# Kernel optimization log

Hardware: AMD Instinct MI355X
Metric: run time of the kernel (lower is better)

The kernel has to match this reference:

```python
import jax, jax.numpy as jnp
import numpy as np

N = 8192
IN_DIM = 512
OUT_DIM = 512


def setup_inputs() -> dict:
    key = jax.random.key(0)
    kA, kX, k1, k2, k3, k4 = jax.random.split(key, 6)
    A = jax.random.uniform(kA, (N, N), dtype=jnp.float32)  # strictly positive -> nonzero triu
    X = jax.random.normal(kX, (N, IN_DIM), dtype=jnp.float32)
    s = 1.0 / np.sqrt(IN_DIM)
    W1 = jax.random.uniform(k1, (OUT_DIM, IN_DIM), minval=-s, maxval=s, dtype=jnp.float32)  # fc
    b1 = jax.random.uniform(k2, (OUT_DIM,), minval=-s, maxval=s, dtype=jnp.float32)
    W2 = jax.random.uniform(k3, (OUT_DIM, IN_DIM), minval=-s, maxval=s, dtype=jnp.float32)  # fc2
    b2 = jax.random.uniform(k4, (OUT_DIM,), minval=-s, maxval=s, dtype=jnp.float32)
    return {"A": A, "X": X, "W1": W1, "b1": b1, "W2": W2, "b2": b2}


def reference(A, X, W1, b1, W2, b2):
    n = A.shape[0]
    # strictly upper-triangular mask (diagonal=1); with uniform(0,1) fill all these
    # entries are nonzero, so torch.nonzero selects exactly them: m = n(n-1)/2 values.
    triu_mask = jnp.triu(jnp.ones((n, n), dtype=bool), k=1)
    m = n * (n - 1) // 2
    # torch.median = lower median = sorted[(m-1)//2]; pad non-triu entries with +inf
    vals = jnp.where(triu_mask, A, jnp.inf).reshape(-1)
    median_value = jnp.sort(vals)[(m - 1) // 2]
    # A[A < median] = 0
    A_thr = jnp.where(A < median_value, jnp.zeros((), A.dtype), A)
    A_norm = jax.nn.softmax(A_thr, axis=-1)
    fcX = X @ W1.T + b1    # [N, out_dim]
    fc2X = X @ W2.T + b2   # [N, out_dim]
    out = jax.nn.leaky_relu(0.1 * fc2X + 0.9 * (A_norm @ fcX), negative_slope=0.01)
    return out
```

## Files before the change

### kernel.cpp

```cpp
#include <hip/hip_runtime.h>

#define DEVI __device__ __forceinline__

typedef __attribute__((ext_vector_type(8))) short short8;
typedef __attribute__((ext_vector_type(4))) float f32x4;

static constexpr int NN = 8192;
static constexpr int DD = 512;
static constexpr unsigned LOB = 0x3EFE0000u;
static constexpr unsigned HIB = 0x3F020000u;
static constexpr long long K_RANK = 16775167LL;

static constexpr size_t WS_HIST = 0;
static constexpr size_t WS_CNT  = 1048576;
static constexpr size_t WS_MED  = 1048832;
static constexpr size_t WS_XB   = 2097152;
static constexpr size_t WS_W1B  = WS_XB  + (size_t)NN * DD * 2;
static constexpr size_t WS_W2B  = WS_W1B + (size_t)DD * DD * 2;
static constexpr size_t WS_FCXT = WS_W2B + (size_t)DD * DD * 2;
static constexpr size_t WS_FC2  = WS_FCXT + (size_t)NN * DD * 2;
static constexpr size_t WS_UP   = WS_FC2 + (size_t)NN * DD * 4;
static constexpr size_t WS_ZP   = WS_UP  + (size_t)4 * NN * DD * 2;

DEVI unsigned short f2bf(float f) {
  unsigned u = __float_as_uint(f);
  u += 0x7fffu + ((u >> 16) & 1u);
  return (unsigned short)(u >> 16);
}
DEVI float bf2f(unsigned short h) { return __uint_as_float(((unsigned)h) << 16); }
DEVI int swz(int row, int kq) { return kq ^ ((row >> 1) & 3); }

DEVI void gl_lds16(const void* g, void* l) {
  __builtin_amdgcn_global_load_lds(
      (const __attribute__((address_space(1))) unsigned*)g,
      (__attribute__((address_space(3))) unsigned*)l, 16, 0, 0);
}

#define VMCNT(n) asm volatile("s_waitcnt vmcnt(" #n ")" ::: "memory")
#define LGKM0 asm volatile("s_waitcnt lgkmcnt(0)" ::: "memory")

__global__ __launch_bounds__(256) void hist_k(const float* __restrict__ A,
                                              unsigned* __restrict__ hist,
                                              unsigned* __restrict__ below) {
  unsigned cnt = 0;
  const long long nt = (long long)gridDim.x * blockDim.x;
  const float4* A4 = (const float4*)A;
  for (long long q = (long long)blockIdx.x * blockDim.x + threadIdx.x; q < 16777216LL; q += nt) {
    long long base = q << 2;
    int row = (int)(base >> 13);
    int col = (int)(base & 8191);
    if (col + 3 <= row) continue;
    float4 v = A4[q];
    float vv[4] = {v.x, v.y, v.z, v.w};
#pragma unroll
    for (int j = 0; j < 4; ++j) {
      if (col + j > row) {
        unsigned u = __float_as_uint(vv[j]);
        if (u < LOB) cnt++;
        else if (u < HIB) atomicAdd(&hist[u - LOB], 1u);
      }
    }
  }
  for (int off = 32; off > 0; off >>= 1) cnt += __shfl_down(cnt, off);
  if ((threadIdx.x & 63) == 0 && cnt) atomicAdd(below, cnt);
}

__global__ __launch_bounds__(1024) void select_k(const unsigned* __restrict__ hist,
                                                 const unsigned* __restrict__ below,
                                                 unsigned* __restrict__ med) {
  __shared__ unsigned ssum[1024];
  __shared__ int owner;
  __shared__ unsigned tg_s;
  const int t = threadIdx.x;
  unsigned own = 0;
#pragma unroll 4
  for (int b = 0; b < 256; ++b) own += hist[t * 256 + b];
  ssum[t] = own;
  __syncthreads();
  for (int off = 1; off < 1024; off <<= 1) {
    unsigned v = (t >= off) ? ssum[t - off] : 0u;
    __syncthreads();
    ssum[t] += v;
    __syncthreads();
  }
  long long target = K_RANK - (long long)(*below);
  unsigned incl = ssum[t];
  unsigned excl = incl - own;
  if (target >= (long long)excl && target < (long long)incl) {
    owner = t;
    tg_s = (unsigned)(target - (long long)excl);
  }
  __syncthreads();
  const int to = owner;
  const unsigned tg = tg_s;
  unsigned v256 = (t < 256) ? hist[to * 256 + t] : 0u;
  __syncthreads();
  if (t < 256) ssum[t] = v256;
  __syncthreads();
  for (int off = 1; off < 256; off <<= 1) {
    unsigned v = (t < 256 && t >= off) ? ssum[t - off] : 0u;
    __syncthreads();
    if (t < 256) ssum[t] += v;
    __syncthreads();
  }
  if (t < 256) {
    unsigned incl2 = ssum[t];
    unsigned excl2 = incl2 - v256;
    if (tg >= excl2 && tg < incl2) *med = LOB + (unsigned)(to * 256 + t);
  }
}

__global__ __launch_bounds__(256) void convert_k(const float* __restrict__ X,
                                                 const float* __restrict__ W1,
                                                 const float* __restrict__ W2,
                                                 unsigned short* __restrict__ Xb,
                                                 unsigned short* __restrict__ W1b,
                                                 unsigned short* __restrict__ W2b) {
  const long long nt = (long long)gridDim.x * blockDim.x;
  const long long NX = (long long)NN * DD;
  const long long NW = (long long)DD * DD;
  for (long long q = (long long)blockIdx.x * blockDim.x + threadIdx.x; q < (NX + 2 * NW) / 4; q += nt) {
    long long e = q << 2;
    const float4* src; unsigned short* dst; long long off;
    if (e < NX)            { src = (const float4*)X;  dst = Xb;  off = e; }
    else if (e < NX + NW)  { src = (const float4*)W1; dst = W1b; off = e - NX; }
    else                   { src = (const float4*)W2; dst = W2b; off = e - NX - NW; }
    float4 v = src[off >> 2];
    ushort4 o;
    o.x = f2bf(v.x); o.y = f2bf(v.y); o.z = f2bf(v.z); o.w = f2bf(v.w);
    *(ushort4*)(dst + off) = o;
  }
}

template <bool BROW, bool OBF>
__global__ __launch_bounds__(512, 2) void gemm_small_k(const unsigned short* __restrict__ Am,
                                                       const unsigned short* __restrict__ Bm,
                                                       const float* __restrict__ bias,
                                                       void* __restrict__ outp, int ldout) {
  __shared__ alignas(16) unsigned short Ap[64 * 32];
  __shared__ alignas(16) unsigned short Bt[256 * 32];
  char* apB = (char*)Ap;
  char* btB = (char*)Bt;
  const int tid = threadIdx.x, lane = tid & 63, w = tid >> 6;
  const int wm = w >> 2, wn = w & 3;
  const int lr = lane & 15, lq = lane >> 4;
  const int m0 = blockIdx.y * 64, n0 = blockIdx.x * 256;
  const int rL = lane >> 2, kq = lane & 3;
  f32x4 acc[2][4];
#pragma unroll
  for (int i = 0; i < 2; ++i)
#pragma unroll
    for (int j = 0; j < 4; ++j) acc[i][j] = (f32x4){0.f, 0.f, 0.f, 0.f};

#pragma unroll 1
  for (int kt = 0; kt < 16; ++kt) {
    const int k0 = kt * 32;
    __syncthreads();
    if (w < 4) {
      int r = w * 16 + rL;
      gl_lds16(Am + ((size_t)(m0 + r) * DD + k0 + swz(r, kq) * 8), apB + w * 1024);
    }
#pragma unroll
    for (int i = 0; i < 2; ++i) {
      int blk = w * 2 + i;
      int r = blk * 16 + rL;
      gl_lds16(Bm + ((size_t)(n0 + r) * DD + k0 + swz(r, kq) * 8), btB + blk * 1024);
    }
    __syncthreads();
    short8 a[2], b[4];
#pragma unroll
    for (int fr = 0; fr < 2; ++fr) {
      int r = wm * 32 + fr * 16 + lr;
      a[fr] = *(const short8*)(apB + r * 64 + swz(r, lq) * 16);
    }
#pragma unroll
    for (int fc = 0; fc < 4; ++fc) {
      int r = wn * 64 + fc * 16 + lr;
      b[fc] = *(const short8*)(btB + r * 64 + swz(r, lq) * 16);
    }
#pragma unroll
    for (int fr = 0; fr < 2; ++fr)
#pragma unroll
      for (int fc = 0; fc < 4; ++fc)
        acc[fr][fc] = __builtin_amdgcn_mfma_f32_16x16x32_bf16(a[fr], b[fc], acc[fr][fc], 0, 0, 0);
  }
#pragma unroll
  for (int fr = 0; fr < 2; ++fr)
#pragma unroll
    for (int fc = 0; fc < 4; ++fc)
#pragma unroll
      for (int j = 0; j < 4; ++j) {
        int row = m0 + wm * 32 + fr * 16 + lq * 4 + j;
        int col = n0 + wn * 64 + fc * 16 + lr;
        float v = acc[fr][fc][j] + (BROW ? bias[row] : bias[col]);
        if (OBF) ((unsigned short*)outp)[(size_t)row * ldout + col] = f2bf(v);
        else     ((float*)outp)[(size_t)row * ldout + col] = v;
      }
}

static constexpr int LDS_A0 = 0;
static constexpr int LDS_A1 = 8192;
static constexpr int LDS_B0 = 16384;
static constexpr int LDS_B1 = 49152;

__global__ __launch_bounds__(512, 2) void main_gemm_k(const float* __restrict__ A,
                                                      const unsigned short* __restrict__ fcXT,
                                                      const unsigned* __restrict__ medp,
                                                      unsigned short* __restrict__ Up,
                                                      float* __restrict__ Zp) {
  __shared__ alignas(16) char lds[81920];
  const int tid = threadIdx.x, lane = tid & 63, w = tid >> 6;
  const int wm = w >> 2, wn = w & 3;
  const int lr = lane & 15, lq = lane >> 4;
  const int ks = blockIdx.x;
  const int m0 = blockIdx.y * 128;
  const int kbase = ks * 2048;
  const float med = __uint_as_float(*medp);
  const int rB = lane >> 2, kqB = lane & 3;
  const int rA = tid >> 2, cqA = tid & 3;
  const float* aRow = A + (size_t)(m0 + rA) * NN;
  const int ldsAw = rA * 64 + swz(rA, cqA) * 16;

  float zacc = 0.f;
  f32x4 acc[4][8];
#pragma unroll
  for (int i = 0; i < 4; ++i)
#pragma unroll
    for (int j = 0; j < 8; ++j) acc[i][j] = (f32x4){0.f, 0.f, 0.f, 0.f};
  float4 vA00, vA01, vA10, vA11;

#define CONV8(V0, V1, DST)                                                     \
  {                                                                            \
    float vv[8] = {V0.x, V0.y, V0.z, V0.w, V1.x, V1.y, V1.z, V1.w};            \
    short8 pb;                                                                 \
    _Pragma("unroll")                                                          \
    for (int j = 0; j < 8; ++j) {                                              \
      float a_ = vv[j];                                                        \
      float p_ = (a_ < med) ? 1.0f : __expf(a_);                               \
      unsigned short h_ = f2bf(p_);                                            \
      pb[j] = (short)h_;                                                       \
      zacc += bf2f(h_);                                                        \
    }                                                                          \
    *(short8*)(DST) = pb;                                                      \
  }

  {
#pragma unroll
    for (int i = 0; i < 4; ++i) {
      int blk = w * 4 + i;
      int o = blk * 16 + rB;
      gl_lds16(fcXT + ((size_t)o * NN + kbase + swz(o, kqB) * 8), lds + LDS_B0 + blk * 1024);
    }
    const float* ap0 = aRow + kbase + cqA * 8;
    float4 t0 = *(const float4*)ap0;
    float4 t1 = *(const float4*)(ap0 + 4);
    vA00 = *(const float4*)(ap0 + 32);
    vA01 = *(const float4*)(ap0 + 36);
    CONV8(t0, t1, lds + LDS_A0 + ldsAw);
  }
  __syncthreads();

#define ITER(KT, CUR, NCUR, VAC0, VAC1, VAN0, VAN1)                            \
  {                                                                            \
    const int kt_ = (KT);                                                      \
    if (kt_ < 63) {                                                            \
      const int k1 = kbase + (kt_ + 1) * 32;                                   \
      _Pragma("unroll")                                                        \
      for (int i = 0; i < 4; ++i) {                                            \
        int blk = w * 4 + i;                                                   \
        int o = blk * 16 + rB;                                                 \
        gl_lds16(fcXT + ((size_t)o * NN + k1 + swz(o, kqB) * 8),               \
                 lds + LDS_B##NCUR + blk * 1024);                              \
      }                                                                        \
      if (kt_ < 62) {                                                          \
        const float* apf = aRow + kbase + (kt_ + 2) * 32 + cqA * 8;            \
        asm volatile("global_load_dwordx4 %0, %2, off\n\t"                     \
                     "global_load_dwordx4 %1, %2, off offset:16"               \
                     : "=&v"(VAN0), "=&v"(VAN1)                                \
                     : "v"(apf)                                                \
                     : "memory");                                              \
      }                                                                        \
    }                                                                          \
    short8 af[4], bfr[8];                                                      \
    _Pragma("unroll")                                                          \
    for (int fr = 0; fr < 4; ++fr) {                                           \
      int r = wm * 64 + fr * 16 + lr;                                          \
      af[fr] = *(const short8*)(lds + LDS_A##CUR + r * 64 + swz(r, lq) * 16);  \
    }                                                                          \
    _Pragma("unroll")                                                          \
    for (int fc = 0; fc < 8; ++fc) {                                           \
      int o = wn * 128 + fc * 16 + lr;                                         \
      bfr[fc] = *(const short8*)(lds + LDS_B##CUR + o * 64 + swz(o, lq) * 16); \
    }                                                                          \
    __builtin_amdgcn_s_setprio(1);                                             \
    _Pragma("unroll")                                                          \
    for (int fr = 0; fr < 4; ++fr)                                             \
      _Pragma("unroll")                                                        \
      for (int fc = 0; fc < 8; ++fc)                                           \
        acc[fr][fc] = __builtin_amdgcn_mfma_f32_16x16x32_bf16(af[fr], bfr[fc], \
                                                              acc[fr][fc], 0, 0, 0); \
    __builtin_amdgcn_s_setprio(0);                                             \
    if (kt_ < 63) {                                                            \
      if (kt_ < 62) { VMCNT(6); } else { VMCNT(4); }                           \
      __builtin_amdgcn_sched_barrier(0);                                       \
      CONV8(VAC0, VAC1, lds + LDS_A##NCUR + ldsAw);                            \
      if (kt_ < 62) { VMCNT(2); } else { VMCNT(0); }                           \
      LGKM0;                                                                   \
      __builtin_amdgcn_s_barrier();                                            \
    }                                                                          \
  }

#pragma unroll 1
  for (int t2 = 0; t2 < 32; ++t2) {
    ITER(2 * t2,     0, 1, vA00, vA01, vA10, vA11);
    ITER(2 * t2 + 1, 1, 0, vA10, vA11, vA00, vA01);
  }
#undef ITER
#undef CONV8

  zacc += __shfl_xor(zacc, 1);
  zacc += __shfl_xor(zacc, 2);
  if ((lane & 3) == 0) Zp[(size_t)ks * NN + m0 + rA] = zacc;
#pragma unroll
  for (int fr = 0; fr < 4; ++fr)
#pragma unroll
    for (int fc = 0; fc < 8; ++fc)
#pragma unroll
      for (int j = 0; j < 4; ++j) {
        int row = m0 + wm * 64 + fr * 16 + lq * 4 + j;
        int col = wn * 128 + fc * 16 + lr;
        Up[((size_t)ks << 22) + ((size_t)row << 9) + col] = f2bf(acc[fr][fc][j]);
      }
}

__global__ __launch_bounds__(256) void reduce_k(const unsigned short* __restrict__ Up,
                                                const float* __restrict__ Zp,
                                                const float* __restrict__ fc2,
                                                float* __restrict__ out) {
  long long t = (long long)blockIdx.x * blockDim.x + threadIdx.x;
  if (t >= (long long)NN * DD / 8) return;
  long long base = t << 3;
  int row = (int)(base >> 9);
  float Z = Zp[row] + Zp[NN + row] + Zp[2 * NN + row] + Zp[3 * NN + row];
  float inv = 0.9f / Z;
  float s[8] = {0, 0, 0, 0, 0, 0, 0, 0};
#pragma unroll
  for (int sp = 0; sp < 4; ++sp) {
    const uint4 u = *(const uint4*)(Up + ((long long)sp << 22) + base);
    const unsigned uu[4] = {u.x, u.y, u.z, u.w};
#pragma unroll
    for (int j = 0; j < 4; ++j) {
      s[2 * j]     += __uint_as_float(uu[j] << 16);
      s[2 * j + 1] += __uint_as_float(uu[j] & 0xffff0000u);
    }
  }
  float4 fa = *(const float4*)(fc2 + base);
  float4 fb = *(const float4*)(fc2 + base + 4);
  float fv[8] = {fa.x, fa.y, fa.z, fa.w, fb.x, fb.y, fb.z, fb.w};
  float o[8];
#pragma unroll
  for (int j = 0; j < 8; ++j) {
    float v = 0.1f * fv[j] + inv * s[j];
    o[j] = v >= 0.f ? v : 0.01f * v;
  }
  *(float4*)(out + base)     = (float4){o[0], o[1], o[2], o[3]};
  *(float4*)(out + base + 4) = (float4){o[4], o[5], o[6], o[7]};
}

extern "C" void kernel_launch(void* const* d_in, const int* in_sizes, int n_in,
                              void* d_out, int out_size, void* d_ws, size_t ws_size,
                              hipStream_t stream) {
  const float* A  = (const float*)d_in[0];
  const float* X  = (const float*)d_in[1];
  const float* W1 = (const float*)d_in[2];
  const float* b1 = (const float*)d_in[3];
  const float* W2 = (const float*)d_in[4];
  const float* b2 = (const float*)d_in[5];
  char* ws = (char*)d_ws;
  unsigned* hist = (unsigned*)(ws + WS_HIST);
  unsigned* cnt  = (unsigned*)(ws + WS_CNT);
  unsigned* med  = (unsigned*)(ws + WS_MED);
  unsigned short* Xb   = (unsigned short*)(ws + WS_XB);
  unsigned short* W1b  = (unsigned short*)(ws + WS_W1B);
  unsigned short* W2b  = (unsigned short*)(ws + WS_W2B);
  unsigned short* fcXT = (unsigned short*)(ws + WS_FCXT);
  float* fc2           = (float*)(ws + WS_FC2);
  unsigned short* Upp  = (unsigned short*)(ws + WS_UP);
  float* Zp            = (float*)(ws + WS_ZP);

  hipMemsetAsync(ws, 0, 1048576 + 512, stream);
  hipLaunchKernelGGL(hist_k, dim3(2048), dim3(256), 0, stream, A, hist, cnt);
  hipLaunchKernelGGL(select_k, dim3(1), dim3(1024), 0, stream, hist, cnt, med);
  hipLaunchKernelGGL(convert_k, dim3(1024), dim3(256), 0, stream, X, W1, W2, Xb, W1b, W2b);
  hipLaunchKernelGGL((gemm_small_k<true, true>), dim3(32, 8), dim3(512), 0, stream,
                     W1b, Xb, b1, (void*)fcXT, NN);
  hipLaunchKernelGGL((gemm_small_k<false, false>), dim3(2, 128), dim3(512), 0, stream,
                     Xb, W2b, b2, (void*)fc2, DD);
  hipLaunchKernelGGL(main_gemm_k, dim3(4, 64), dim3(512), 0, stream, A, fcXT, med, Upp, Zp);
  hipLaunchKernelGGL(reduce_k, dim3(2048), dim3(256), 0, stream, Upp, Zp, fc2, (float*)d_out);
}
```

Measured before the change: 293.6 us.

## Fuse histogram and small GEMMs into one prep kernel, halve main GEMM tile

The histogram pass and both small projection GEMMs now run as block ranges of a single prep kernel. The GEMMs convert fp32 to bf16 inline while loading, so the separate convert kernel and its workspace buffers go away. The main GEMM drops from 128 to 64 rows per block, doubling the grid and raising launch bounds to 4 blocks per CU for more occupancy and better CU fill. The select kernel also reads the histogram with vectorised uint4 loads. In exchange, the GEMMs lose the async global-to-LDS path, and the smaller main tile re-reads fcX more often.

```diff
diff --git a/kernel.cpp b/kernel.cpp
--- a/kernel.cpp
+++ b/kernel.cpp
@@ -3,6 +3,7 @@
 #define DEVI __device__ __forceinline__
 
 typedef __attribute__((ext_vector_type(8))) short short8;
+typedef __attribute__((ext_vector_type(4))) short short4v;
 typedef __attribute__((ext_vector_type(4))) float f32x4;
 
 static constexpr int NN = 8192;
@@ -14,10 +15,7 @@
 static constexpr size_t WS_HIST = 0;
 static constexpr size_t WS_CNT  = 1048576;
 static constexpr size_t WS_MED  = 1048832;
-static constexpr size_t WS_XB   = 2097152;
-static constexpr size_t WS_W1B  = WS_XB  + (size_t)NN * DD * 2;
-static constexpr size_t WS_W2B  = WS_W1B + (size_t)DD * DD * 2;
-static constexpr size_t WS_FCXT = WS_W2B + (size_t)DD * DD * 2;
+static constexpr size_t WS_FCXT = 2097152;
 static constexpr size_t WS_FC2  = WS_FCXT + (size_t)NN * DD * 2;
 static constexpr size_t WS_UP   = WS_FC2 + (size_t)NN * DD * 4;
 static constexpr size_t WS_ZP   = WS_UP  + (size_t)4 * NN * DD * 2;
@@ -39,13 +37,12 @@
 #define VMCNT(n) asm volatile("s_waitcnt vmcnt(" #n ")" ::: "memory")
 #define LGKM0 asm volatile("s_waitcnt lgkmcnt(0)" ::: "memory")
 
-__global__ __launch_bounds__(256) void hist_k(const float* __restrict__ A,
-                                              unsigned* __restrict__ hist,
-                                              unsigned* __restrict__ below) {
+
+DEVI void hist_body(const float* __restrict__ A, unsigned* __restrict__ hist,
+                    unsigned* __restrict__ below, int hb, int tid) {
   unsigned cnt = 0;
-  const long long nt = (long long)gridDim.x * blockDim.x;
   const float4* A4 = (const float4*)A;
-  for (long long q = (long long)blockIdx.x * blockDim.x + threadIdx.x; q < 16777216LL; q += nt) {
+  for (long long q = (long long)hb * 512 + tid; q < 16777216LL; q += 524288LL) {
     long long base = q << 2;
     int row = (int)(base >> 13);
     int col = (int)(base & 8191);
@@ -62,7 +59,104 @@
     }
   }
   for (int off = 32; off > 0; off >>= 1) cnt += __shfl_down(cnt, off);
-  if ((threadIdx.x & 63) == 0 && cnt) atomicAdd(below, cnt);
+  if ((tid & 63) == 0 && cnt) atomicAdd(below, cnt);
+}
+
+template <bool BROW, bool OBF>
+DEVI void gemm_body(const float* __restrict__ Am, const float* __restrict__ Bm,
+                    const float* __restrict__ bias, void* __restrict__ outp, int ldout,
+                    int m0, int n0, char* apB, char* btB) {
+  const int tid = threadIdx.x, lane = tid & 63, w = tid >> 6;
+  const int wm = w >> 2, wn = w & 3;
+  const int lr = lane & 15, lq = lane >> 4;
+  f32x4 acc[2][4];
+#pragma unroll
+  for (int i = 0; i < 2; ++i)
+#pragma unroll
+    for (int j = 0; j < 4; ++j) acc[i][j] = (f32x4){0.f, 0.f, 0.f, 0.f};
+
+  const int arow = tid >> 3, acq = tid & 7;
+  const int brow = tid >> 1, bhalf = tid & 1;
+
+#pragma unroll 1
+  for (int kt = 0; kt < 16; ++kt) {
+    const int k0 = kt * 32;
+    __syncthreads();
+    {
+      float4 v = *(const float4*)(Am + (size_t)(m0 + arow) * DD + k0 + acq * 4);
+      short4v o;
+      o[0] = (short)f2bf(v.x); o[1] = (short)f2bf(v.y);
+      o[2] = (short)f2bf(v.z); o[3] = (short)f2bf(v.w);
+      *(short4v*)(apB + arow * 64 + swz(arow, acq >> 1) * 16 + (acq & 1) * 8) = o;
+    }
+    {
+      const float* bp = Bm + (size_t)(n0 + brow) * DD + k0 + bhalf * 16;
+      float4 v0 = *(const float4*)bp;
+      float4 v1 = *(const float4*)(bp + 4);
+      float4 v2 = *(const float4*)(bp + 8);
+      float4 v3 = *(const float4*)(bp + 12);
+      float vv[16] = {v0.x, v0.y, v0.z, v0.w, v1.x, v1.y, v1.z, v1.w,
+                      v2.x, v2.y, v2.z, v2.w, v3.x, v3.y, v3.z, v3.w};
+      short8 s0, s1;
+#pragma unroll
+      for (int j = 0; j < 8; ++j) { s0[j] = (short)f2bf(vv[j]); s1[j] = (short)f2bf(vv[8 + j]); }
+      *(short8*)(btB + brow * 64 + swz(brow, bhalf * 2) * 16) = s0;
+      *(short8*)(btB + brow * 64 + swz(brow, bhalf * 2 + 1) * 16) = s1;
+    }
+    __syncthreads();
+    short8 a[2], b[4];
+#pragma unroll
+    for (int fr = 0; fr < 2; ++fr) {
+      int r = wm * 32 + fr * 16 + lr;
+      a[fr] = *(const short8*)(apB + r * 64 + swz(r, lq) * 16);
+    }
+#pragma unroll
+    for (int fc = 0; fc < 4; ++fc) {
+      int r = wn * 64 + fc * 16 + lr;
+      b[fc] = *(const short8*)(btB + r * 64 + swz(r, lq) * 16);
+    }
+#pragma unroll
+    for (int fr = 0; fr < 2; ++fr)
+#pragma unroll
+      for (int fc = 0; fc < 4; ++fc)
+        acc[fr][fc] = __builtin_amdgcn_mfma_f32_16x16x32_bf16(a[fr], b[fc], acc[fr][fc], 0, 0, 0);
+  }
+#pragma unroll
+  for (int fr = 0; fr < 2; ++fr)
+#pragma unroll
+    for (int fc = 0; fc < 4; ++fc)
+#pragma unroll
+      for (int j = 0; j < 4; ++j) {
+        int row = m0 + wm * 32 + fr * 16 + lq * 4 + j;
+        int col = n0 + wn * 64 + fc * 16 + lr;
+        float v = acc[fr][fc][j] + (BROW ? bias[row] : bias[col]);
+        if (OBF) ((unsigned short*)outp)[(size_t)row * ldout + col] = f2bf(v);
+        else     ((float*)outp)[(size_t)row * ldout + col] = v;
+      }
+}
+
+__global__ __launch_bounds__(512) void prep_k(const float* __restrict__ A,
+                                              const float* __restrict__ X,
+                                              const float* __restrict__ W1,
+                                              const float* __restrict__ b1,
+                                              const float* __restrict__ W2,
+                                              const float* __restrict__ b2,
+                                              unsigned* __restrict__ hist,
+                                              unsigned* __restrict__ below,
+                                              unsigned short* __restrict__ fcXT,
+                                              float* __restrict__ fc2) {
+  __shared__ alignas(16) char plds[20480];
+  const int bx = blockIdx.x;
+  if (bx >= 512) {
+    hist_body(A, hist, below, bx - 512, threadIdx.x);
+  } else if (bx < 256) {
+    gemm_body<true, true>(W1, X, b1, (void*)fcXT, NN,
+                          (bx >> 5) * 64, (bx & 31) * 256, plds, plds + 4096);
+  } else {
+    int q = bx - 256;
+    gemm_body<false, false>(X, W2, b2, (void*)fc2, DD,
+                            (q >> 1) * 64, (q & 1) * 256, plds, plds + 4096);
+  }
 }
 
 __global__ __launch_bounds__(1024) void select_k(const unsigned* __restrict__ hist,
@@ -73,8 +167,12 @@
   __shared__ unsigned tg_s;
   const int t = threadIdx.x;
   unsigned own = 0;
-#pragma unroll 4
-  for (int b = 0; b < 256; ++b) own += hist[t * 256 + b];
+  const uint4* h4 = (const uint4*)(hist + t * 256);
+#pragma unroll 8
+  for (int b = 0; b < 64; ++b) {
+    uint4 v = h4[b];
+    own += v.x + v.y + v.z + v.w;
+  }
   ssum[t] = own;
   __syncthreads();
   for (int off = 1; off < 1024; off <<= 1) {
@@ -110,138 +208,50 @@
   }
 }
 
-__global__ __launch_bounds__(256) void convert_k(const float* __restrict__ X,
-                                                 const float* __restrict__ W1,
-                                                 const float* __restrict__ W2,
-                                                 unsigned short* __restrict__ Xb,
-                                                 unsigned short* __restrict__ W1b,
-                                                 unsigned short* __restrict__ W2b) {
-  const long long nt = (long long)gridDim.x * blockDim.x;
-  const long long NX = (long long)NN * DD;
-  const long long NW = (long long)DD * DD;
-  for (long long q = (long long)blockIdx.x * blockDim.x + threadIdx.x; q < (NX + 2 * NW) / 4; q += nt) {
-    long long e = q << 2;
-    const float4* src; unsigned short* dst; long long off;
-    if (e < NX)            { src = (const float4*)X;  dst = Xb;  off = e; }
-    else if (e < NX + NW)  { src = (const float4*)W1; dst = W1b; off = e - NX; }
-    else                   { src = (const float4*)W2; dst = W2b; off = e - NX - NW; }
-    float4 v = src[off >> 2];
-    ushort4 o;
-    o.x = f2bf(v.x); o.y = f2bf(v.y); o.z = f2bf(v.z); o.w = f2bf(v.w);
-    *(ushort4*)(dst + off) = o;
-  }
-}
-
-template <bool BROW, bool OBF>
-__global__ __launch_bounds__(512, 2) void gemm_small_k(const unsigned short* __restrict__ Am,
-                                                       const unsigned short* __restrict__ Bm,
-                                                       const float* __restrict__ bias,
-                                                       void* __restrict__ outp, int ldout) {
-  __shared__ alignas(16) unsigned short Ap[64 * 32];
-  __shared__ alignas(16) unsigned short Bt[256 * 32];
-  char* apB = (char*)Ap;
-  char* btB = (char*)Bt;
-  const int tid = threadIdx.x, lane = tid & 63, w = tid >> 6;
-  const int wm = w >> 2, wn = w & 3;
-  const int lr = lane & 15, lq = lane >> 4;
-  const int m0 = blockIdx.y * 64, n0 = blockIdx.x * 256;
-  const int rL = lane >> 2, kq = lane & 3;
-  f32x4 acc[2][4];
-#pragma unroll
-  for (int i = 0; i < 2; ++i)
-#pragma unroll
-    for (int j = 0; j < 4; ++j) acc[i][j] = (f32x4){0.f, 0.f, 0.f, 0.f};
-
-#pragma unroll 1
-  for (int kt = 0; kt < 16; ++kt) {
-    const int k0 = kt * 32;
-    __syncthreads();
-    if (w < 4) {
-      int r = w * 16 + rL;
-      gl_lds16(Am + ((size_t)(m0 + r) * DD + k0 + swz(r, kq) * 8), apB + w * 1024);
-    }
-#pragma unroll
-    for (int i = 0; i < 2; ++i) {
-      int blk = w * 2 + i;
-      int r = blk * 16 + rL;
-      gl_lds16(Bm + ((size_t)(n0 + r) * DD + k0 + swz(r, kq) * 8), btB + blk * 1024);
-    }
-    __syncthreads();
-    short8 a[2], b[4];
-#pragma unroll
-    for (int fr = 0; fr < 2; ++fr) {
-      int r = wm * 32 + fr * 16 + lr;
-      a[fr] = *(const short8*)(apB + r * 64 + swz(r, lq) * 16);
-    }
-#pragma unroll
-    for (int fc = 0; fc < 4; ++fc) {
-      int r = wn * 64 + fc * 16 + lr;
-      b[fc] = *(const short8*)(btB + r * 64 + swz(r, lq) * 16);
-    }
-#pragma unroll
-    for (int fr = 0; fr < 2; ++fr)
-#pragma unroll
-      for (int fc = 0; fc < 4; ++fc)
-        acc[fr][fc] = __builtin_amdgcn_mfma_f32_16x16x32_bf16(a[fr], b[fc], acc[fr][fc], 0, 0, 0);
-  }
-#pragma unroll
-  for (int fr = 0; fr < 2; ++fr)
-#pragma unroll
-    for (int fc = 0; fc < 4; ++fc)
-#pragma unroll
-      for (int j = 0; j < 4; ++j) {
-        int row = m0 + wm * 32 + fr * 16 + lq * 4 + j;
-        int col = n0 + wn * 64 + fc * 16 + lr;
-        float v = acc[fr][fc][j] + (BROW ? bias[row] : bias[col]);
-        if (OBF) ((unsigned short*)outp)[(size_t)row * ldout + col] = f2bf(v);
-        else     ((float*)outp)[(size_t)row * ldout + col] = v;
-      }
-}
-
 static constexpr int LDS_A0 = 0;
-static constexpr int LDS_A1 = 8192;
-static constexpr int LDS_B0 = 16384;
-static constexpr int LDS_B1 = 49152;
-
-__global__ __launch_bounds__(512, 2) void main_gemm_k(const float* __restrict__ A,
+static constexpr int LDS_A1 = 4096;
+static constexpr int LDS_B0 = 8192;
+static constexpr int LDS_B1 = 40960;
+
+__global__ __launch_bounds__(512, 4) void main_gemm_k(const float* __restrict__ A,
                                                       const unsigned short* __restrict__ fcXT,
                                                       const unsigned* __restrict__ medp,
                                                       unsigned short* __restrict__ Up,
                                                       float* __restrict__ Zp) {
-  __shared__ alignas(16) char lds[81920];
+  __shared__ alignas(16) char lds[73728];
   const int tid = threadIdx.x, lane = tid & 63, w = tid >> 6;
   const int wm = w >> 2, wn = w & 3;
   const int lr = lane & 15, lq = lane >> 4;
   const int ks = blockIdx.x;
-  const int m0 = blockIdx.y * 128;
+  const int m0 = blockIdx.y * 64;
   const int kbase = ks * 2048;
   const float med = __uint_as_float(*medp);
   const int rB = lane >> 2, kqB = lane & 3;
-  const int rA = tid >> 2, cqA = tid & 3;
+  const int rA = tid >> 3, cqA = tid & 7;
   const float* aRow = A + (size_t)(m0 + rA) * NN;
-  const int ldsAw = rA * 64 + swz(rA, cqA) * 16;
+  const int ldsAw = rA * 64 + swz(rA, cqA >> 1) * 16 + (cqA & 1) * 8;
 
   float zacc = 0.f;
-  f32x4 acc[4][8];
-#pragma unroll
-  for (int i = 0; i < 4; ++i)
+  f32x4 acc[2][8];
+#pragma unroll
+  for (int i = 0; i < 2; ++i)
 #pragma unroll
     for (int j = 0; j < 8; ++j) acc[i][j] = (f32x4){0.f, 0.f, 0.f, 0.f};
-  float4 vA00, vA01, vA10, vA11;
-
-#define CONV8(V0, V1, DST)                                                     \
+  float4 vA0, vA1;
+
+#define CONV4(V, DST)                                                          \
   {                                                                            \
-    float vv[8] = {V0.x, V0.y, V0.z, V0.w, V1.x, V1.y, V1.z, V1.w};            \
-    short8 pb;                                                                 \
+    float vv[4] = {V.x, V.y, V.z, V.w};                                        \
+    short4v pb;                                                                \
     _Pragma("unroll")                                                          \
-    for (int j = 0; j < 8; ++j) {                                              \
+    for (int j = 0; j < 4; ++j) {                                              \
       float a_ = vv[j];                                                        \
       float p_ = (a_ < med) ? 1.0f : __expf(a_);                               \
       unsigned short h_ = f2bf(p_);                                            \
       pb[j] = (short)h_;                                                       \
       zacc += bf2f(h_);                                                        \
     }                                                                          \
-    *(short8*)(DST) = pb;                                                      \
+    *(short4v*)(DST) = pb;                                                     \
   }
 
   {
@@ -251,16 +261,13 @@
       int o = blk * 16 + rB;
       gl_lds16(fcXT + ((size_t)o * NN + kbase + swz(o, kqB) * 8), lds + LDS_B0 + blk * 1024);
     }
-    const float* ap0 = aRow + kbase + cqA * 8;
-    float4 t0 = *(const float4*)ap0;
-    float4 t1 = *(const float4*)(ap0 + 4);
-    vA00 = *(const float4*)(ap0 + 32);
-    vA01 = *(const float4*)(ap0 + 36);
-    CONV8(t0, t1, lds + LDS_A0 + ldsAw);
-  }
-  __syncthreads();
-
-#define ITER(KT, CUR, NCUR, VAC0, VAC1, VAN0, VAN1)                            \
+    float4 t0 = *(const float4*)(aRow + kbase + cqA * 4);
+    vA0 = *(const float4*)(aRow + kbase + 32 + cqA * 4);
+    CONV4(t0, lds + LDS_A0 + ldsAw);
+  }
+  __syncthreads();
+
+#define ITER(KT, CUR, NCUR, VAC, VAN)                                          \
   {                                                                            \
     const int kt_ = (KT);                                                      \
     if (kt_ < 63) {                                                            \
@@ -273,18 +280,15 @@
                  lds + LDS_B##NCUR + blk * 1024);                              \
       }                                                                        \
       if (kt_ < 62) {                                                          \
-        const float* apf = aRow + kbase + (kt_ + 2) * 32 + cqA * 8;            \
-        asm volatile("global_load_dwordx4 %0, %2, off\n\t"                     \
-                     "global_load_dwordx4 %1, %2, off offset:16"               \
-                     : "=&v"(VAN0), "=&v"(VAN1)                                \
-                     : "v"(apf)                                                \
-                     : "memory");                                              \
+        const float* apf = aRow + kbase + (kt_ + 2) * 32 + cqA * 4;            \
+        asm volatile("global_load_dwordx4 %0, %1, off"                         \
+                     : "=&v"(VAN) : "v"(apf) : "memory");                      \
       }                                                                        \
     }                                                                          \
-    short8 af[4], bfr[8];                                                      \
+    short8 af[2], bfr[8];                                                      \
     _Pragma("unroll")                                                          \
-    for (int fr = 0; fr < 4; ++fr) {                                           \
-      int r = wm * 64 + fr * 16 + lr;                                          \
+    for (int fr = 0; fr < 2; ++fr) {                                           \
+      int r = wm * 32 + fr * 16 + lr;                                          \
       af[fr] = *(const short8*)(lds + LDS_A##CUR + r * 64 + swz(r, lq) * 16);  \
     }                                                                          \
     _Pragma("unroll")                                                          \
@@ -294,17 +298,17 @@
     }                                                                          \
     __builtin_amdgcn_s_setprio(1);                                             \
     _Pragma("unroll")                                                          \
-    for (int fr = 0; fr < 4; ++fr)                                             \
+    for (int fr = 0; fr < 2; ++fr)                                             \
       _Pragma("unroll")                                                        \
       for (int fc = 0; fc < 8; ++fc)                                           \
         acc[fr][fc] = __builtin_amdgcn_mfma_f32_16x16x32_bf16(af[fr], bfr[fc], \
                                                               acc[fr][fc], 0, 0, 0); \
     __builtin_amdgcn_s_setprio(0);                                             \
     if (kt_ < 63) {                                                            \
-      if (kt_ < 62) { VMCNT(6); } else { VMCNT(4); }                           \
+      if (kt_ < 62) { VMCNT(5); } else { VMCNT(4); }                           \
       __builtin_amdgcn_sched_barrier(0);                                       \
-      CONV8(VAC0, VAC1, lds + LDS_A##NCUR + ldsAw);                            \
-      if (kt_ < 62) { VMCNT(2); } else { VMCNT(0); }                           \
+      CONV4(VAC, lds + LDS_A##NCUR + ldsAw);                                   \
+      if (kt_ < 62) { VMCNT(1); } else { VMCNT(0); }                           \
       LGKM0;                                                                   \
       __builtin_amdgcn_s_barrier();                                            \
     }                                                                          \
@@ -312,22 +316,23 @@
 
 #pragma unroll 1
   for (int t2 = 0; t2 < 32; ++t2) {
-    ITER(2 * t2,     0, 1, vA00, vA01, vA10, vA11);
-    ITER(2 * t2 + 1, 1, 0, vA10, vA11, vA00, vA01);
+    ITER(2 * t2,     0, 1, vA0, vA1);
+    ITER(2 * t2 + 1, 1, 0, vA1, vA0);
   }
 #undef ITER
-#undef CONV8
+#undef CONV4
 
   zacc += __shfl_xor(zacc, 1);
   zacc += __shfl_xor(zacc, 2);
-  if ((lane & 3) == 0) Zp[(size_t)ks * NN + m0 + rA] = zacc;
-#pragma unroll
-  for (int fr = 0; fr < 4; ++fr)
+  zacc += __shfl_xor(zacc, 4);
+  if ((tid & 7) == 0) Zp[(size_t)ks * NN + m0 + rA] = zacc;
+#pragma unroll
+  for (int fr = 0; fr < 2; ++fr)
 #pragma unroll
     for (int fc = 0; fc < 8; ++fc)
 #pragma unroll
       for (int j = 0; j < 4; ++j) {
-        int row = m0 + wm * 64 + fr * 16 + lq * 4 + j;
+        int row = m0 + wm * 32 + fr * 16 + lq * 4 + j;
         int col = wn * 128 + fc * 16 + lr;
         Up[((size_t)ks << 22) + ((size_t)row << 9) + col] = f2bf(acc[fr][fc][j]);
       }
@@ -380,22 +385,15 @@
   unsigned* hist = (unsigned*)(ws + WS_HIST);
   unsigned* cnt  = (unsigned*)(ws + WS_CNT);
   unsigned* med  = (unsigned*)(ws + WS_MED);
-  unsigned short* Xb   = (unsigned short*)(ws + WS_XB);
-  unsigned short* W1b  = (unsigned short*)(ws + WS_W1B);
-  unsigned short* W2b  = (unsigned short*)(ws + WS_W2B);
   unsigned short* fcXT = (unsigned short*)(ws + WS_FCXT);
   float* fc2           = (float*)(ws + WS_FC2);
   unsigned short* Upp  = (unsigned short*)(ws + WS_UP);
   float* Zp            = (float*)(ws + WS_ZP);
 
   hipMemsetAsync(ws, 0, 1048576 + 512, stream);
-  hipLaunchKernelGGL(hist_k, dim3(2048), dim3(256), 0, stream, A, hist, cnt);
+  hipLaunchKernelGGL(prep_k, dim3(1536), dim3(512), 0, stream,
+                     A, X, W1, b1, W2, b2, hist, cnt, fcXT, fc2);
   hipLaunchKernelGGL(select_k, dim3(1), dim3(1024), 0, stream, hist, cnt, med);
-  hipLaunchKernelGGL(convert_k, dim3(1024), dim3(256), 0, stream, X, W1, W2, Xb, W1b, W2b);
-  hipLaunchKernelGGL((gemm_small_k<true, true>), dim3(32, 8), dim3(512), 0, stream,
-                     W1b, Xb, b1, (void*)fcXT, NN);
-  hipLaunchKernelGGL((gemm_small_k<false, false>), dim3(2, 128), dim3(512), 0, stream,
-                     Xb, W2b, b2, (void*)fc2, DD);
-  hipLaunchKernelGGL(main_gemm_k, dim3(4, 64), dim3(512), 0, stream, A, fcXT, med, Upp, Zp);
+  hipLaunchKernelGGL(main_gemm_k, dim3(4, 128), dim3(512), 0, stream, A, fcXT, med, Upp, Zp);
   hipLaunchKernelGGL(reduce_k, dim3(2048), dim3(256), 0, stream, Upp, Zp, fc2, (float*)d_out);
 }
```

Measured after the change: 398.4 us. 35.7% more time.
